# Optimization experiments

Hardware: AMD Instinct MI355X
Metric: run time of the kernel (lower is better)

Reference implementation:

```python
import jax, jax.numpy as jnp
import numpy as np

N_NODES = 128   # num_nodes
BATCH = 4096
HIDDEN = 32     # fixed by the module's Linear(N+1, 32)


def setup_inputs() -> dict:
    key = jax.random.key(0)
    ks = jax.random.split(key, 8)
    N, B, H = N_NODES, BATCH, HIDDEN
    x = jax.random.normal(ks[0], (B, N), dtype=jnp.float32)
    # adjacency masks: A[b, :, j] = parent indicator of node j in sample b
    A = (jax.random.uniform(ks[1], (B, N, N)) < 0.3).astype(jnp.float32)
    # per-sample topological permutation
    order = jax.vmap(lambda k: jax.random.permutation(k, N))(
        jax.random.split(ks[2], B)).astype(jnp.int32)
    # intervention target per sample, -1 = no intervention
    do_idxs = jax.random.randint(ks[3], (B,), -1, N, dtype=jnp.int32)
    # externalized intervention noise (torch.normal in the original forward)
    u = jax.random.normal(ks[4], (B,), dtype=jnp.float32)
    # stacked per-node MLP params: Linear(N+1, 32) -> LeakyReLU -> Linear(32, 1)
    W1 = jax.random.normal(ks[5], (N, N + 1, H), dtype=jnp.float32) / np.sqrt(N + 1)
    b1 = jnp.zeros((N, H), dtype=jnp.float32)
    W2 = jax.random.normal(ks[6], (N, H, 1), dtype=jnp.float32) / np.sqrt(H)
    b2 = jnp.zeros((N, 1), dtype=jnp.float32)
    return dict(x=x, A=A, u=u, W1=W1, b1=b1, W2=W2, b2=b2,
                order=order, do_idxs=do_idxs)


def reference(x, A, u, W1, b1, W2, b2, order, do_idxs):
    B, N = x.shape
    bidx = jnp.arange(B)
    # set intervened entries: outputs[b, do_idxs[b]] = u[b] where do_idxs != -1
    outputs0 = jnp.where(do_idxs[:, None] == jnp.arange(N)[None, :],
                         u[:, None], jnp.zeros_like(x))

    def step(outputs, node):           # node: [B] current node per sample
        mask = A[bidx, :, node]        # [B, N] parent mask of this node
        ins = jnp.concatenate([mask * outputs,
                               x[bidx, node][:, None]], axis=1)  # [B, N+1]
        # per-node MLP gathered by node id (grouped tiny GEMMs)
        h = jax.nn.leaky_relu(jnp.einsum('bd,bdh->bh', ins, W1[node]) + b1[node])
        out = (jnp.einsum('bh,bho->bo', h, W2[node]) + b2[node])[:, 0]  # [B]
        # intervened samples keep their value u (they are skipped in the original)
        new_val = jnp.where(do_idxs == node, outputs[bidx, node], out)
        return outputs.at[bidx, node].set(new_val), None

    outputs, _ = jax.lax.scan(step, outputs0, order.T)  # sequential topo order
    return outputs
```

## Files before the change

### kernel.cpp

```cpp
#include <hip/hip_runtime.h>
#include <stdint.h>

#define NN 128
#define BB 4096
#define HH 32

__global__ __launch_bounds__(256) void pack_bits(const float* __restrict__ A,
                                                 ulonglong2* __restrict__ bitsT) {
    int tid = blockIdx.x * 256 + threadIdx.x;
    int b = tid >> 7;
    int node = tid & 127;
    const float* Ab = A + (size_t)b * NN * NN + node;
    unsigned long long w0 = 0, w1 = 0;
#pragma unroll 8
    for (int d = 0; d < 64; ++d) {
        float v = __builtin_nontemporal_load(&Ab[d * NN]);
        if (v != 0.f) w0 |= 1ull << d;
    }
#pragma unroll 8
    for (int d = 0; d < 64; ++d) {
        float v = __builtin_nontemporal_load(&Ab[(d + 64) * NN]);
        if (v != 0.f) w1 |= 1ull << d;
    }
    ulonglong2 r; r.x = w0; r.y = w1;
    bitsT[tid] = r;
}

__global__ __launch_bounds__(64) void cond_mlp(
    const float* __restrict__ x, const float* __restrict__ u,
    const float* __restrict__ W1, const float* __restrict__ b1,
    const float* __restrict__ W2, const float* __restrict__ b2,
    const int* __restrict__ order, const int* __restrict__ do_idxs,
    const ulonglong2* __restrict__ bitsT, float* __restrict__ out)
{
    const int b = blockIdx.x;
    const int lane = threadIdx.x;
    const int j = lane & 31;
    const int half = lane >> 5;

    __shared__ float2 ent[132];

    const float ub = u[b];
    const int dob = do_idxs[b];
    float out0 = (dob == lane) ? ub : 0.f;
    float out1 = (dob == lane + 64) ? ub : 0.f;

    const int* ord = order + b * NN;
    const ulonglong2* bb = bitsT + (size_t)b * NN;

    int node = ord[0];
    ulonglong2 bits = bb[node];

    for (int t = 0; t < NN; ++t) {
        const int node_n = (t < NN - 1) ? ord[t + 1] : 0;
        const ulonglong2 bits_n = bb[node_n];

        const float* Wn = W1 + (size_t)node * (NN + 1) * HH;
        const float w2v = W2[node * HH + j];
        const float b1v = b1[node * HH + j];
        const float xv  = x[b * NN + node];
        const float b2v = b2[node];

        unsigned long long bal0 = __ballot(out0 != 0.f) & bits.x;
        unsigned long long bal1 = __ballot(out1 != 0.f) & bits.y;
        const int c0 = __popcll(bal0);
        const int cnt = c0 + __popcll(bal1);
        const unsigned long long below = (1ull << lane) - 1;
        if (bal0 & (1ull << lane)) {
            int p = __popcll(bal0 & below);
            ent[p] = make_float2(out0, __int_as_float(lane));
        }
        if (bal1 & (1ull << lane)) {
            int p = c0 + __popcll(bal1 & below);
            ent[p] = make_float2(out1, __int_as_float(lane + 64));
        }
        const int cnt4 = (cnt + 3) & ~3;
        if (lane < cnt4 - cnt) ent[cnt + lane] = make_float2(0.f, __int_as_float(0));
        __syncthreads();

        float acc0 = 0.f, acc1 = 0.f;
        for (int k = 0; k < cnt4; k += 4) {
            float2 eA = ent[k + half];
            float2 eB = ent[k + 2 + half];
            int dA = __float_as_int(eA.y);
            int dB = __float_as_int(eB.y);
            acc0 += eA.x * Wn[dA * HH + j];
            acc1 += eB.x * Wn[dB * HH + j];
        }
        __syncthreads();

        float acc = acc0 + acc1;
        acc += __shfl_xor(acc, 32);
        acc += xv * Wn[NN * HH + j];
        acc += b1v;
        const float hv = (acc > 0.f) ? acc : 0.01f * acc;

        float p = hv * w2v;
        p += __shfl_xor(p, 16);
        p += __shfl_xor(p, 8);
        p += __shfl_xor(p, 4);
        p += __shfl_xor(p, 2);
        p += __shfl_xor(p, 1);
        const float outv = p + b2v;

        if (dob != node) {
            if (lane == (node & 63)) {
                if (node < 64) out0 = outv; else out1 = outv;
            }
        }
        node = node_n;
        bits = bits_n;
    }

    out[b * NN + lane] = out0;
    out[b * NN + 64 + lane] = out1;
}

extern "C" void kernel_launch(void* const* d_in, const int* in_sizes, int n_in,
                              void* d_out, int out_size, void* d_ws, size_t ws_size,
                              hipStream_t stream) {
    const float* x   = (const float*)d_in[0];
    const float* A   = (const float*)d_in[1];
    const float* u   = (const float*)d_in[2];
    const float* W1  = (const float*)d_in[3];
    const float* b1  = (const float*)d_in[4];
    const float* W2  = (const float*)d_in[5];
    const float* b2  = (const float*)d_in[6];
    const int* order = (const int*)d_in[7];
    const int* dox   = (const int*)d_in[8];

    ulonglong2* bitsT = (ulonglong2*)d_ws;

    pack_bits<<<(BB * NN) / 256, 256, 0, stream>>>(A, bitsT);
    cond_mlp<<<BB, 64, 0, stream>>>(x, u, W1, b1, W2, b2, order, dox,
                                    bitsT, (float*)d_out);
}
```

Baseline: 540.7 us.

## Prefetch per-node params via registers, drop block barriers, vectorize bit packing

Each block now preloads the order, parent bitmasks, x and b2 rows into registers once, and fetches them per step with wave shuffles instead of scalar global loads. The next node's W2, b1 and x-weight values are software-prefetched one step ahead. Because the block is a single 64-wide wavefront, the __syncthreads calls are replaced by an LDS waitcnt. The stored parent index is pre-scaled by HH, and part of the output reduction uses DPP instead of shuffles. pack_bits now has each thread load float4 across four nodes, cutting its thread count by four. The risks are extra register pressure and reliance on single-wave semantics for LDS ordering.

```diff
diff --git a/kernel.cpp b/kernel.cpp
--- a/kernel.cpp
+++ b/kernel.cpp
@@ -5,25 +5,40 @@
 #define BB 4096
 #define HH 32
 
+typedef float f4 __attribute__((ext_vector_type(4)));
+
 __global__ __launch_bounds__(256) void pack_bits(const float* __restrict__ A,
                                                  ulonglong2* __restrict__ bitsT) {
-    int tid = blockIdx.x * 256 + threadIdx.x;
-    int b = tid >> 7;
-    int node = tid & 127;
-    const float* Ab = A + (size_t)b * NN * NN + node;
-    unsigned long long w0 = 0, w1 = 0;
+    const int tid = blockIdx.x * 256 + threadIdx.x;
+    const int b   = tid >> 5;
+    const int ng  = (tid & 31) << 2;
+    const float* Ab = A + (size_t)b * (NN * NN) + ng;
+    unsigned long long w0[4] = {0ull, 0ull, 0ull, 0ull};
+    unsigned long long w1[4] = {0ull, 0ull, 0ull, 0ull};
 #pragma unroll 8
     for (int d = 0; d < 64; ++d) {
-        float v = __builtin_nontemporal_load(&Ab[d * NN]);
-        if (v != 0.f) w0 |= 1ull << d;
+        f4 v = __builtin_nontemporal_load((const f4*)(Ab + (size_t)d * NN));
+        const unsigned long long bit = 1ull << d;
+        if (v[0] != 0.f) w0[0] |= bit;
+        if (v[1] != 0.f) w0[1] |= bit;
+        if (v[2] != 0.f) w0[2] |= bit;
+        if (v[3] != 0.f) w0[3] |= bit;
     }
 #pragma unroll 8
     for (int d = 0; d < 64; ++d) {
-        float v = __builtin_nontemporal_load(&Ab[(d + 64) * NN]);
-        if (v != 0.f) w1 |= 1ull << d;
+        f4 v = __builtin_nontemporal_load((const f4*)(Ab + (size_t)(d + 64) * NN));
+        const unsigned long long bit = 1ull << d;
+        if (v[0] != 0.f) w1[0] |= bit;
+        if (v[1] != 0.f) w1[1] |= bit;
+        if (v[2] != 0.f) w1[2] |= bit;
+        if (v[3] != 0.f) w1[3] |= bit;
     }
-    ulonglong2 r; r.x = w0; r.y = w1;
-    bitsT[tid] = r;
+    ulonglong2* o = bitsT + b * NN + ng;
+#pragma unroll
+    for (int i = 0; i < 4; ++i) {
+        ulonglong2 r; r.x = w0[i]; r.y = w1[i];
+        o[i] = r;
+    }
 }
 
 __global__ __launch_bounds__(64) void cond_mlp(
@@ -46,37 +61,55 @@
     float out1 = (dob == lane + 64) ? ub : 0.f;
 
     const int* ord = order + b * NN;
-    const ulonglong2* bb = bitsT + (size_t)b * NN;
+    const int orA = ord[lane];
+    const int orB = ord[lane + 64];
+    const ulonglong2 B0 = bitsT[(size_t)b * NN + lane];
+    const ulonglong2 B1 = bitsT[(size_t)b * NN + 64 + lane];
+    const float xr0 = x[b * NN + lane];
+    const float xr1 = x[b * NN + 64 + lane];
+    const float b2r0 = b2[lane];
+    const float b2r1 = b2[lane + 64];
 
-    int node = ord[0];
-    ulonglong2 bits = bb[node];
+    const unsigned long long lanebit = 1ull << lane;
+    const unsigned long long below = lanebit - 1ull;
+
+    int node = __builtin_amdgcn_readfirstlane(__shfl(orA, 0));
+    unsigned long long bitsx = __shfl((node & 64) ? B1.x : B0.x, node & 63);
+    unsigned long long bitsy = __shfl((node & 64) ? B1.y : B0.y, node & 63);
+    const float* Wn = W1 + (size_t)node * ((NN + 1) * HH);
+    float w2v  = W2[node * HH + j];
+    float b1v  = b1[node * HH + j];
+    float w1xv = Wn[NN * HH + j];
 
     for (int t = 0; t < NN; ++t) {
-        const int node_n = (t < NN - 1) ? ord[t + 1] : 0;
-        const ulonglong2 bits_n = bb[node_n];
+        const int nsel = (t + 1) & 127;
+        const int node_n = __builtin_amdgcn_readfirstlane(
+            __shfl((nsel & 64) ? orB : orA, nsel & 63));
+        const unsigned long long bx_n = __shfl((node_n & 64) ? B1.x : B0.x, node_n & 63);
+        const unsigned long long by_n = __shfl((node_n & 64) ? B1.y : B0.y, node_n & 63);
+        const float* Wn_n = W1 + (size_t)node_n * ((NN + 1) * HH);
+        const float w2v_n  = W2[node_n * HH + j];
+        const float b1v_n  = b1[node_n * HH + j];
+        const float w1xv_n = Wn_n[NN * HH + j];
 
-        const float* Wn = W1 + (size_t)node * (NN + 1) * HH;
-        const float w2v = W2[node * HH + j];
-        const float b1v = b1[node * HH + j];
-        const float xv  = x[b * NN + node];
-        const float b2v = b2[node];
+        const float xv  = __shfl((node & 64) ? xr1 : xr0, node & 63);
+        const float b2v = __shfl((node & 64) ? b2r1 : b2r0, node & 63);
 
-        unsigned long long bal0 = __ballot(out0 != 0.f) & bits.x;
-        unsigned long long bal1 = __ballot(out1 != 0.f) & bits.y;
+        unsigned long long bal0 = __ballot(out0 != 0.f) & bitsx;
+        unsigned long long bal1 = __ballot(out1 != 0.f) & bitsy;
         const int c0 = __popcll(bal0);
         const int cnt = c0 + __popcll(bal1);
-        const unsigned long long below = (1ull << lane) - 1;
-        if (bal0 & (1ull << lane)) {
+        if (bal0 & lanebit) {
             int p = __popcll(bal0 & below);
-            ent[p] = make_float2(out0, __int_as_float(lane));
+            ent[p] = make_float2(out0, __int_as_float(lane << 5));
         }
-        if (bal1 & (1ull << lane)) {
+        if (bal1 & lanebit) {
             int p = c0 + __popcll(bal1 & below);
-            ent[p] = make_float2(out1, __int_as_float(lane + 64));
+            ent[p] = make_float2(out1, __int_as_float((lane + 64) << 5));
         }
         const int cnt4 = (cnt + 3) & ~3;
         if (lane < cnt4 - cnt) ent[cnt + lane] = make_float2(0.f, __int_as_float(0));
-        __syncthreads();
+        asm volatile("s_waitcnt lgkmcnt(0)" ::: "memory");
 
         float acc0 = 0.f, acc1 = 0.f;
         for (int k = 0; k < cnt4; k += 4) {
@@ -84,32 +117,34 @@
             float2 eB = ent[k + 2 + half];
             int dA = __float_as_int(eA.y);
             int dB = __float_as_int(eB.y);
-            acc0 += eA.x * Wn[dA * HH + j];
-            acc1 += eB.x * Wn[dB * HH + j];
+            acc0 += eA.x * Wn[dA + j];
+            acc1 += eB.x * Wn[dB + j];
         }
-        __syncthreads();
 
         float acc = acc0 + acc1;
         acc += __shfl_xor(acc, 32);
-        acc += xv * Wn[NN * HH + j];
+        acc += xv * w1xv;
         acc += b1v;
         const float hv = (acc > 0.f) ? acc : 0.01f * acc;
 
         float p = hv * w2v;
+        p += __int_as_float(__builtin_amdgcn_update_dpp(
+                 0, __float_as_int(p), 0xB1, 0xF, 0xF, true));
+        p += __int_as_float(__builtin_amdgcn_update_dpp(
+                 0, __float_as_int(p), 0x4E, 0xF, 0xF, true));
+        p += __int_as_float(__builtin_amdgcn_update_dpp(
+                 0, __float_as_int(p), 0x141, 0xF, 0xF, true));
+        p += __int_as_float(__builtin_amdgcn_update_dpp(
+                 0, __float_as_int(p), 0x140, 0xF, 0xF, true));
         p += __shfl_xor(p, 16);
-        p += __shfl_xor(p, 8);
-        p += __shfl_xor(p, 4);
-        p += __shfl_xor(p, 2);
-        p += __shfl_xor(p, 1);
         const float outv = p + b2v;
 
-        if (dob != node) {
-            if (lane == (node & 63)) {
-                if (node < 64) out0 = outv; else out1 = outv;
-            }
+        if (dob != node && lane == (node & 63)) {
+            if (node < 64) out0 = outv; else out1 = outv;
         }
-        node = node_n;
-        bits = bits_n;
+
+        node = node_n; bitsx = bx_n; bitsy = by_n;
+        Wn = Wn_n; w2v = w2v_n; b1v = b1v_n; w1xv = w1xv_n;
     }
 
     out[b * NN + lane] = out0;
@@ -131,7 +166,7 @@
 
     ulonglong2* bitsT = (ulonglong2*)d_ws;
 
-    pack_bits<<<(BB * NN) / 256, 256, 0, stream>>>(A, bitsT);
+    pack_bits<<<(BB * 32) / 256, 256, 0, stream>>>(A, bitsT);
     cond_mlp<<<BB, 64, 0, stream>>>(x, u, W1, b1, W2, b2, order, dox,
                                     bitsT, (float*)d_out);
 }
```

Result: slower. 661.3 us (+22.3%).
